# Kernel optimization log

Measured on AMD Instinct MI355X. Metric: run time of the kernel, lower is better.

## Reference

```python
import jax, jax.numpy as jnp
from jax import lax
import numpy as np

H, W, C = 128, 128, 1024          # backbone feature map (stride-16, ResNet C4)
STRIDE = 16
NUM_ANCHORS = 9                   # 3 scales x 3 ratios
IOU_THRESHOLD = 0.7
SCORE_THRESHOLD = 0.5


def _make_anchors():
    scales = np.array([128.0, 256.0, 512.0], np.float32)
    ratios = np.array([0.5, 1.0, 2.0], np.float32)
    hs = (scales[:, None] * np.sqrt(ratios)[None, :]).reshape(-1)   # [9]
    ws = (scales[:, None] / np.sqrt(ratios)[None, :]).reshape(-1)   # [9]
    cy = (np.arange(H, dtype=np.float32) + 0.5) * STRIDE
    cx = (np.arange(W, dtype=np.float32) + 0.5) * STRIDE
    anc = np.zeros((H, W, NUM_ANCHORS, 4), np.float32)
    anc[..., 0] = cy[:, None, None]
    anc[..., 1] = cx[None, :, None]
    anc[..., 2] = hs
    anc[..., 3] = ws
    return anc.reshape(-1, 4)      # [N,4] as (cy, cx, h, w)


def _conv(x, w, b):
    return lax.conv_general_dilated(
        x, w, (1, 1), 'SAME', dimension_numbers=('NHWC', 'HWIO', 'NHWC')) + b


def _rpn_head(features, w1, b1, w2, b2, w_score, b_score, w_box, b_box):
    x = jax.nn.relu(features)
    x = _conv(x, w1, b1)
    x = jax.nn.relu(x)
    x = _conv(x, w2, b2)
    scores = jax.nn.sigmoid(_conv(x, w_score, b_score))   # [1,H,W,9]
    shifts = _conv(x, w_box, b_box)                        # [1,H,W,36]
    return scores.reshape(-1, 1), shifts.reshape(-1, 4)


def _decode(shifts, anchors):
    acy, acx, ah, aw = anchors[:, 0], anchors[:, 1], anchors[:, 2], anchors[:, 3]
    dy, dx, dh, dw = shifts[:, 0], shifts[:, 1], shifts[:, 2], shifts[:, 3]
    cy = acy + dy * ah
    cx = acx + dx * aw
    h = ah * jnp.exp(dh)
    w = aw * jnp.exp(dw)
    y1 = jnp.clip(cy - 0.5 * h, 0.0, H * STRIDE)
    x1 = jnp.clip(cx - 0.5 * w, 0.0, W * STRIDE)
    y2 = jnp.clip(cy + 0.5 * h, 0.0, H * STRIDE)
    x2 = jnp.clip(cx + 0.5 * w, 0.0, W * STRIDE)
    return jnp.stack([y1, x1, y2, x2], axis=-1)            # [N,4]


def _nms(boxes, scores, max_out):
    """Greedy NMS like tf.image.non_max_suppression, fixed-size padded output."""
    n = boxes.shape[0]
    areas = (boxes[:, 2] - boxes[:, 0]) * (boxes[:, 3] - boxes[:, 1])

    def body(state):
        suppressed, sel, count = state
        masked = jnp.where(suppressed, -jnp.inf, scores)
        i = jnp.argmax(masked)
        valid = masked[i] >= SCORE_THRESHOLD
        sel = sel.at[count].set(jnp.where(valid, i.astype(jnp.int32), -1))
        count = count + valid.astype(jnp.int32)
        b = boxes[i]
        iy = jnp.maximum(0.0, jnp.minimum(b[2], boxes[:, 2]) - jnp.maximum(b[0], boxes[:, 0]))
        ix = jnp.maximum(0.0, jnp.minimum(b[3], boxes[:, 3]) - jnp.maximum(b[1], boxes[:, 1]))
        inter = iy * ix
        iou = inter / (areas[i] + areas - inter + 1e-9)
        new_sup = (suppressed | (iou > IOU_THRESHOLD)).at[i].set(True)
        suppressed = jnp.where(valid, new_sup, jnp.ones_like(suppressed))
        return suppressed, sel, count

    def cond(state):
        suppressed, sel, count = state
        return (count < max_out) & (~jnp.all(suppressed))

    sel0 = jnp.full((max_out,), -1, jnp.int32)
    sup0 = jnp.zeros((n,), bool)
    _, sel, _ = lax.while_loop(cond, body, (sup0, sel0, jnp.int32(0)))
    valid = sel >= 0
    idx = jnp.where(valid, sel, 0)
    return boxes[idx] * valid[:, None], scores[idx] * valid, valid


def setup_inputs() -> dict:
    key = jax.random.key(0)
    ks = jax.random.split(key, 5)
    def init_w(k, shape, fan_in, scale=1.0):
        return jax.random.normal(k, shape, jnp.float32) * (scale / np.sqrt(fan_in))
    features = jax.random.normal(ks[0], (1, H, W, C), jnp.float32)
    w1 = init_w(ks[1], (3, 3, C, 512), 9 * C)
    b1 = jnp.zeros((512,), jnp.float32)
    w2 = init_w(ks[2], (3, 3, 512, 512), 9 * 512)
    b2 = jnp.zeros((512,), jnp.float32)
    w_score = init_w(ks[3], (1, 1, 512, NUM_ANCHORS), 512)
    b_score = jnp.zeros((NUM_ANCHORS,), jnp.float32)
    w_box = init_w(ks[4], (1, 1, 512, 4 * NUM_ANCHORS), 512, scale=0.1)
    b_box = jnp.zeros((4 * NUM_ANCHORS,), jnp.float32)
    return {"features": features, "w1": w1, "b1": b1, "w2": w2, "b2": b2,
            "w_score": w_score, "b_score": b_score,
            "w_box": w_box, "b_box": b_box, "region_limit": 300}


def reference(features, w1, b1, w2, b2, w_score, b_score, w_box, b_box, region_limit):
    pred_scores, pred_shifts = _rpn_head(features, w1, b1, w2, b2,
                                         w_score, b_score, w_box, b_box)
    anchors = jnp.asarray(_make_anchors())
    boxes = _decode(pred_shifts, anchors)
    return _nms(boxes, pred_scores[:, 0], int(region_limit))
```

## Files before the change

kernel.cpp:

```cpp
#include <hip/hip_runtime.h>

#define HW 128
#define COUTC 512
#define NB 4097
#define NSEL 300
#define T_TOP 4096
#define TW 64

typedef _Float16 half8 __attribute__((ext_vector_type(8)));
typedef _Float16 half4v __attribute__((ext_vector_type(4)));
typedef float floatx4 __attribute__((ext_vector_type(4)));

#define NWS_A1H   ((size_t)0)
#define NWS_A1L   ((size_t)34611200)
#define NWS_W1H   ((size_t)69222400)
#define NWS_W1L   ((size_t)78659584)
#define NWS_A2H   ((size_t)88096768)
#define NWS_A2L   ((size_t)105402368)
#define NWS_W2H   ((size_t)122707968)
#define NWS_W2L   ((size_t)127426560)
#define NWS_X2    ((size_t)132145152)
#define NWS_BOXES ((size_t)165699584)
#define NWS_KEYS  ((size_t)168058880)
#define NWS_SKEYS ((size_t)169238528)
#define NWS_HIST  ((size_t)170418176)
#define NWS_CUR   ((size_t)170434816)
#define NWS_CNT   ((size_t)170451456)
#define NWS_BASE  ((size_t)170451712)
#define NWS_TOTAL ((size_t)170468352)

#define WS_X1     ((size_t)0)
#define WS_X2     ((size_t)33554432)
#define WS_BOXES  ((size_t)67108864)
#define WS_KEYS   ((size_t)69468160)
#define WS_SKEYS  ((size_t)70647808)
#define WS_HIST   ((size_t)71827456)
#define WS_CUR    ((size_t)71844096)
#define WS_CNT    ((size_t)71860736)
#define WS_BASE   ((size_t)71860992)

__device__ __forceinline__ void glds16(const void* g, void* l) {
    __builtin_amdgcn_global_load_lds(
        (const __attribute__((address_space(1))) void*)g,
        (__attribute__((address_space(3))) void*)l, 16, 0, 0);
}


__global__ __launch_bounds__(256) void convert_feat_kernel(
    const float* __restrict__ feat, _Float16* __restrict__ ah, _Float16* __restrict__ al)
{
    int p  = blockIdx.x;
    int pr = p / 130, pc = p % 130;
    int c  = threadIdx.x * 4;
    half4v vh = (half4v)(_Float16)0.f, vl = (half4v)(_Float16)0.f;
    if (pr != 0 && pr != 129 && pc != 0 && pc != 129) {
        float4 v = *(const float4*)&feat[(size_t)(((pr - 1) * HW) + (pc - 1)) * 1024 + c];
        float f[4] = {v.x, v.y, v.z, v.w};
        #pragma unroll
        for (int i = 0; i < 4; ++i) {
            float x = fmaxf(f[i], 0.f);
            _Float16 hi = (_Float16)x;
            vh[i] = hi;
            vl[i] = (_Float16)(x - (float)hi);
        }
    }
    size_t o = (size_t)pr * 133120 + (size_t)(c >> 5) * 4160
             + (size_t)((c >> 3) & 3) * 1040 + (size_t)pc * 8 + (c & 7);
    *(half4v*)&ah[o] = vh;
    *(half4v*)&al[o] = vl;
}

template<int CIN>
__device__ __forceinline__ void convert_w_body(
    int b, const float* __restrict__ w, _Float16* __restrict__ wh, _Float16* __restrict__ wl)
{
    constexpr int NU = CIN / 8;
    int gid = b * 256 + threadIdx.x;
    int oc = gid & 511;
    int rest = gid >> 9;
    int u = rest & (NU - 1);
    int tap = rest / NU;
    if (tap >= 9) return;
    int k0 = u * 8;
    half8 vh, vl;
    #pragma unroll
    for (int j = 0; j < 8; ++j) {
        float v = w[((size_t)tap * CIN + k0 + j) * 512 + oc] * 64.f;
        _Float16 hi = (_Float16)v;
        vh[j] = hi;
        vl[j] = (_Float16)(v - (float)hi);
    }
    size_t o = (size_t)tap * CIN * 512 + (size_t)(k0 >> 5) * 16384
             + (size_t)((k0 >> 3) & 3) * 4096 + (size_t)oc * 8;
    *(half8*)(wh + o) = vh;
    *(half8*)(wl + o) = vl;
}

__global__ __launch_bounds__(256) void prep_kernel(
    const float* __restrict__ w1, _Float16* __restrict__ w1h, _Float16* __restrict__ w1l,
    const float* __restrict__ w2, _Float16* __restrict__ w2h, _Float16* __restrict__ w2l,
    const float* __restrict__ w_s, const float* __restrict__ w_b,
    _Float16* __restrict__ wbh, _Float16* __restrict__ wbl,
    _Float16* __restrict__ a2h, _Float16* __restrict__ a2l)
{
    int b = blockIdx.x;
    if (b < 2304) { convert_w_body<1024>(b, w1, w1h, w1l); return; }
    if (b < 3456) { convert_w_body<512>(b - 2304, w2, w2h, w2l); return; }
    if (b < 3584) {
        int gid = (b - 3456) * 256 + threadIdx.x;
        int n = gid & 63;
        int k = gid >> 6;
        float v = 0.f;
        if (n < 9)       v = w_s[k * 9 + n] * 64.f;
        else if (n < 45) v = w_b[k * 36 + (n - 9)] * 64.f;
        _Float16 hi = (_Float16)v;
        size_t o = (size_t)(k >> 5) * 2048 + (size_t)((k >> 3) & 3) * 512 + (size_t)n * 8 + (k & 7);
        wbh[o] = hi;
        wbl[o] = (_Float16)(v - (float)hi);
        return;
    }
    {
        int i = b - 3584;
        int pr, pc;
        if (i < 130)      { pr = 0;        pc = i; }
        else if (i < 260) { pr = 129;      pc = i - 130; }
        else if (i < 388) { pr = i - 259;  pc = 0; }
        else              { pr = i - 387;  pc = 129; }
        int t = threadIdx.x;
        if (t >= 128) return;
        _Float16* dst = (t & 64) ? a2l : a2h;
        int u = t & 63;
        size_t o = (size_t)pr * 66560 + (size_t)(u >> 2) * 4160 + (size_t)(u & 3) * 1040 + (size_t)pc * 8;
        *(float4*)(dst + o) = make_float4(0.f, 0.f, 0.f, 0.f);
    }
}

template<int CIN, bool PAD>
__global__ __launch_bounds__(256) void conv_mfma_kernel(
    const _Float16* __restrict__ ah, const _Float16* __restrict__ al,
    const _Float16* __restrict__ wh, const _Float16* __restrict__ wl,
    const float* __restrict__ bias,
    _Float16* __restrict__ oh, _Float16* __restrict__ ol)
{
    constexpr int ROWSTR = CIN * 130;
    constexpr int TAPW   = CIN * 512;
    __shared__ __align__(16) _Float16 lds[32768];

    int bx = blockIdx.x;
    int h  = bx & 127;
    int n0 = (bx >> 7) << 7;

    int tid  = threadIdx.x;
    int wave = tid >> 6;
    int lane = tid & 63;
    int fr = lane & 15;
    int fq = lane >> 4;

    int aoff0 = fq * 1040 + (32 * wave + fr) * 8;
    int aoff1 = aoff0 + 128;
    int boff0 = fq * 4096 + (n0 + 32 * wave + fr) * 8;
    int boff1 = boff0 + 128;

    int wm = wave & 1, wn = wave >> 1;

    floatx4 acc[4][4];
    #pragma unroll
    for (int i = 0; i < 4; ++i)
        #pragma unroll
        for (int j = 0; j < 4; ++j)
            acc[i][j] = (floatx4){0.f, 0.f, 0.f, 0.f};

    #pragma unroll
    for (int tap = 0; tap < 9; ++tap) {
        int dy = tap / 3 - 1, dx = tap % 3 - 1;
        const _Float16* gAh = ah + (size_t)(h + dy + 1) * ROWSTR + (dx + 1) * 8;
        const _Float16* gAl = al + (size_t)(h + dy + 1) * ROWSTR + (dx + 1) * 8;
        const _Float16* gBh = wh + (size_t)tap * TAPW;
        const _Float16* gBl = wl + (size_t)tap * TAPW;

        for (int kc = 0; kc < CIN; kc += 64) {
            #pragma unroll
            for (int s = 0; s < 2; ++s) {
                int ab = ((kc >> 5) + s) * 4160;
                int bb = ((kc >> 5) + s) * 16384;
                _Float16* A0 = lds +          s * 4096 + 2 * wave * 512;
                _Float16* L0 = lds + 8192  +  s * 4096 + 2 * wave * 512;
                _Float16* B0 = lds + 16384 +  s * 4096 + 2 * wave * 512;
                _Float16* C0 = lds + 24576 +  s * 4096 + 2 * wave * 512;
                glds16(gAh + ab + aoff0, A0);
                glds16(gAh + ab + aoff1, A0 + 512);
                glds16(gAl + ab + aoff0, L0);
                glds16(gAl + ab + aoff1, L0 + 512);
                glds16(gBh + bb + boff0, B0);
                glds16(gBh + bb + boff1, B0 + 512);
                glds16(gBl + bb + boff0, C0);
                glds16(gBl + bb + boff1, C0 + 512);
            }
            __syncthreads();

            #pragma unroll
            for (int s = 0; s < 2; ++s) {
                const _Float16* rAh = lds +          s * 4096 + wm * 2048 + fq * 128 + fr * 8;
                const _Float16* rAl = rAh + 8192;
                const _Float16* rBh = lds + 16384 +  s * 4096 + wn * 2048 + fq * 128 + fr * 8;
                const _Float16* rBl = rBh + 8192;

                half8 fah[4], fal[4], fbh[4], fbl[4];
                #pragma unroll
                for (int i = 0; i < 4; ++i) {
                    fah[i] = *(const half8*)(rAh + i * 512);
                    fal[i] = *(const half8*)(rAl + i * 512);
                    fbh[i] = *(const half8*)(rBh + i * 512);
                    fbl[i] = *(const half8*)(rBl + i * 512);
                }
                #pragma unroll
                for (int i = 0; i < 4; ++i)
                    #pragma unroll
                    for (int j = 0; j < 4; ++j)
                        acc[i][j] = __builtin_amdgcn_mfma_f32_16x16x32_f16(fah[i], fbh[j], acc[i][j], 0, 0, 0);
                #pragma unroll
                for (int i = 0; i < 4; ++i)
                    #pragma unroll
                    for (int j = 0; j < 4; ++j)
                        acc[i][j] = __builtin_amdgcn_mfma_f32_16x16x32_f16(fah[i], fbl[j], acc[i][j], 0, 0, 0);
                #pragma unroll
                for (int i = 0; i < 4; ++i)
                    #pragma unroll
                    for (int j = 0; j < 4; ++j)
                        acc[i][j] = __builtin_amdgcn_mfma_f32_16x16x32_f16(fal[i], fbh[j], acc[i][j], 0, 0, 0);
            }
            __syncthreads();
        }
    }

    const float scale = 1.f / 64.f;
    int em = 64 * wm + fq * 4;
    int en = 64 * wn + fr;
    #pragma unroll
    for (int j = 0; j < 4; ++j) {
        int oc = n0 + en + 16 * j;
        float b = bias[oc];
        #pragma unroll
        for (int i = 0; i < 4; ++i) {
            #pragma unroll
            for (int r = 0; r < 4; ++r) {
                int w = em + 16 * i + r;
                float v = fmaf(acc[i][j][r], scale, b);
                if (PAD) {
                    v = fmaxf(v, 0.f);
                    _Float16 hi = (_Float16)v;
                    size_t o = (size_t)(h + 1) * 66560 + (size_t)(oc >> 5) * 4160
                             + (size_t)((oc >> 3) & 3) * 1040 + (size_t)(w + 1) * 8 + (oc & 7);
                    oh[o] = hi;
                    ol[o] = (_Float16)(v - (float)hi);
                } else {
                    _Float16 hi = (_Float16)v;
                    size_t o = (size_t)h * 65536 + (size_t)(oc >> 5) * 4096
                             + (size_t)((oc >> 3) & 3) * 1024 + (size_t)w * 8 + (oc & 7);
                    oh[o] = hi;
                    ol[o] = (_Float16)(v - (float)hi);
                }
            }
        }
    }
}

__device__ __forceinline__ void decode_emit(
    int gi, float z, float dyv, float dxv, float dhv, float dwv,
    float4* __restrict__ boxes, unsigned long long* __restrict__ keys,
    int* __restrict__ cnt, int* __restrict__ hist)
{
    int a = gi % 9;
    int pix = gi / 9;
    int h = pix >> 7, w = pix & 127;
    float sc  = (a < 3) ? 128.f : ((a < 6) ? 256.f : 512.f);
    int r = a - (a / 3) * 3;
    float ratio = (r == 0) ? 0.5f : ((r == 1) ? 1.f : 2.f);
    float sr = sqrtf(ratio);
    float ahh = sc * sr, aww = sc / sr;
    float acy = ((float)h + 0.5f) * 16.f;
    float acx = ((float)w + 0.5f) * 16.f;
    float cy = fmaf(dyv, ahh, acy);
    float cx = fmaf(dxv, aww, acx);
    float hh = ahh * expf(dhv);
    float ww = aww * expf(dwv);
    float y1 = fminf(fmaxf(cy - 0.5f * hh, 0.f), 2048.f);
    float x1 = fminf(fmaxf(cx - 0.5f * ww, 0.f), 2048.f);
    float y2 = fminf(fmaxf(cy + 0.5f * hh, 0.f), 2048.f);
    float x2 = fminf(fmaxf(cx + 0.5f * ww, 0.f), 2048.f);
    boxes[gi] = make_float4(y1, x1, y2, x2);
    float s = 1.f / (1.f + expf(-z));
    if (s >= 0.5f) {
        unsigned u = __float_as_uint(s);
        unsigned d = 0x3F800000u - u;
        unsigned long long key = ((unsigned long long)d << 18) | (unsigned)gi;
        int p = atomicAdd(cnt, 1);
        keys[p] = key;
        atomicAdd(&hist[d >> 11], 1);
    }
}

__global__ __launch_bounds__(256) void heads_mfma_kernel(
    const _Float16* __restrict__ xh, const _Float16* __restrict__ xl,
    const _Float16* __restrict__ wbh, const _Float16* __restrict__ wbl,
    const float* __restrict__ b_s, const float* __restrict__ b_b,
    float4* __restrict__ boxes, unsigned long long* __restrict__ keys,
    int* __restrict__ cnt, int* __restrict__ hist)
{
    __shared__ __align__(16) char smem[49152];
    _Float16* sAh = (_Float16*)smem;
    _Float16* sAl = (_Float16*)(smem + 16384);
    _Float16* sBh = (_Float16*)(smem + 32768);
    _Float16* sBl = (_Float16*)(smem + 40960);
    float* outs = (float*)smem;
    __shared__ float sb[48];

    int tid  = threadIdx.x;
    int wave = tid >> 6;
    int lane = tid & 63;
    int fr = lane & 15;
    int fq = lane >> 4;
    if (tid < 48) sb[tid] = (tid < 9) ? b_s[tid] : ((tid < 45) ? b_b[tid - 9] : 0.f);

    int h0 = blockIdx.x << 1;
    int rowsel = wave >> 1;
    int seg = (wave & 1) * 2048;

    floatx4 acc[4][3];
    #pragma unroll
    for (int i = 0; i < 4; ++i)
        #pragma unroll
        for (int j = 0; j < 3; ++j)
            acc[i][j] = (floatx4){0.f, 0.f, 0.f, 0.f};

    for (int kc = 0; kc < 16; ++kc) {
        const _Float16* gxh = xh + (size_t)(h0 + rowsel) * 65536 + kc * 4096 + seg;
        const _Float16* gxl = xl + (size_t)(h0 + rowsel) * 65536 + kc * 4096 + seg;
        _Float16* dAh = sAh + rowsel * 4096 + seg;
        _Float16* dAl = sAl + rowsel * 4096 + seg;
        #pragma unroll
        for (int q = 0; q < 4; ++q) {
            glds16(gxh + q * 512 + lane * 8, dAh + q * 512);
            glds16(gxl + q * 512 + lane * 8, dAl + q * 512);
        }
        glds16(wbh + kc * 2048 + wave * 512 + lane * 8, sBh + wave * 512);
        glds16(wbl + kc * 2048 + wave * 512 + lane * 8, sBl + wave * 512);
        __syncthreads();

        half8 fah[4], fal[4], fbh[3], fbl[3];
        #pragma unroll
        for (int i = 0; i < 4; ++i) {
            int pixLocal = wave * 64 + 16 * i + fr;
            int aaddr = (pixLocal >> 7) * 4096 + fq * 1024 + (pixLocal & 127) * 8;
            fah[i] = *(const half8*)(sAh + aaddr);
            fal[i] = *(const half8*)(sAl + aaddr);
        }
        #pragma unroll
        for (int j = 0; j < 3; ++j) {
            int baddr = fq * 512 + (16 * j + fr) * 8;
            fbh[j] = *(const half8*)(sBh + baddr);
            fbl[j] = *(const half8*)(sBl + baddr);
        }
        #pragma unroll
        for (int i = 0; i < 4; ++i)
            #pragma unroll
            for (int j = 0; j < 3; ++j) {
                acc[i][j] = __builtin_amdgcn_mfma_f32_16x16x32_f16(fah[i], fbh[j], acc[i][j], 0, 0, 0);
                acc[i][j] = __builtin_amdgcn_mfma_f32_16x16x32_f16(fah[i], fbl[j], acc[i][j], 0, 0, 0);
                acc[i][j] = __builtin_amdgcn_mfma_f32_16x16x32_f16(fal[i], fbh[j], acc[i][j], 0, 0, 0);
            }
        __syncthreads();
    }

    const float scale = 1.f / 64.f;
    #pragma unroll
    for (int i = 0; i < 4; ++i)
        #pragma unroll
        for (int j = 0; j < 3; ++j)
            #pragma unroll
            for (int r = 0; r < 4; ++r) {
                int pixLocal = wave * 64 + 16 * i + fq * 4 + r;
                int n = 16 * j + fr;
                if (n < 48)
                    outs[pixLocal * 48 + n] = fmaf(acc[i][j][r], scale, sb[n]);
            }
    __syncthreads();

    int p = tid;
    #pragma unroll
    for (int a = 0; a < 9; ++a) {
        float z   = outs[p * 48 + a];
        float dyv = outs[p * 48 + 9 + 4 * a + 0];
        float dxv = outs[p * 48 + 9 + 4 * a + 1];
        float dhv = outs[p * 48 + 9 + 4 * a + 2];
        float dwv = outs[p * 48 + 9 + 4 * a + 3];
        int gi = (h0 * 128 + p) * 9 + a;
        decode_emit(gi, z, dyv, dxv, dhv, dwv, boxes, keys, cnt, hist);
    }
}

template<int CIN, bool RELU_IN, bool RELU_OUT>
__global__ __launch_bounds__(256) void conv3x3_kernel(
    const float* __restrict__ in, const float* __restrict__ wgt,
    const float* __restrict__ bias, float* __restrict__ out)
{
    __shared__ float As[32][68];
    __shared__ float Bs[32][64];
    int bx = blockIdx.x;
    int mtile = bx & 255, ntile = bx >> 8;
    int h = mtile >> 1, w0 = (mtile & 1) << 6, n0 = ntile << 6;
    int tid = threadIdx.x, ty = tid >> 4, tx = tid & 15;
    float acc[4][4] = {{0.f}};
    const int KTOT = 9 * CIN;
    for (int k0 = 0; k0 < KTOT; k0 += 32) {
        int tap = k0 / CIN, icb = k0 % CIN;
        int dy = tap / 3 - 1, dx = tap % 3 - 1;
        int row = h + dy;
        bool rowok = ((unsigned)row < HW);
        {
            int pix = tid >> 3, cs = (tid & 7) << 2;
            #pragma unroll
            for (int p = 0; p < 2; ++p) {
                int px = pix + p * 32;
                int wcol = w0 + px + dx;
                float4 v = make_float4(0.f, 0.f, 0.f, 0.f);
                if (rowok && (unsigned)wcol < HW) {
                    v = *(const float4*)&in[((size_t)row * HW + wcol) * CIN + icb + cs];
                    if (RELU_IN) {
                        v.x = fmaxf(v.x, 0.f); v.y = fmaxf(v.y, 0.f);
                        v.z = fmaxf(v.z, 0.f); v.w = fmaxf(v.w, 0.f);
                    }
                }
                As[cs + 0][px] = v.x; As[cs + 1][px] = v.y;
                As[cs + 2][px] = v.z; As[cs + 3][px] = v.w;
            }
        }
        {
            int kr = tid >> 4, nc = (tid & 15) << 2;
            #pragma unroll
            for (int p = 0; p < 2; ++p) {
                int k = kr + p * 16;
                *(float4*)&Bs[k][nc] = *(const float4*)&wgt[(size_t)(k0 + k) * COUTC + n0 + nc];
            }
        }
        __syncthreads();
        #pragma unroll
        for (int kk = 0; kk < 32; ++kk) {
            float4 a = *(const float4*)&As[kk][ty << 2];
            float4 b = *(const float4*)&Bs[kk][tx << 2];
            float av[4] = {a.x, a.y, a.z, a.w};
            float bv[4] = {b.x, b.y, b.z, b.w};
            #pragma unroll
            for (int i = 0; i < 4; ++i)
                #pragma unroll
                for (int j = 0; j < 4; ++j)
                    acc[i][j] = fmaf(av[i], bv[j], acc[i][j]);
        }
        __syncthreads();
    }
    float4 bi = *(const float4*)&bias[n0 + (tx << 2)];
    float bv2[4] = {bi.x, bi.y, bi.z, bi.w};
    #pragma unroll
    for (int i = 0; i < 4; ++i) {
        float4 o;
        o.x = acc[i][0] + bv2[0]; o.y = acc[i][1] + bv2[1];
        o.z = acc[i][2] + bv2[2]; o.w = acc[i][3] + bv2[3];
        if (RELU_OUT) {
            o.x = fmaxf(o.x, 0.f); o.y = fmaxf(o.y, 0.f);
            o.z = fmaxf(o.z, 0.f); o.w = fmaxf(o.w, 0.f);
        }
        *(float4*)&out[((size_t)(h * HW) + w0 + (ty << 2) + i) * COUTC + n0 + (tx << 2)] = o;
    }
}

__global__ __launch_bounds__(256) void heads_decode_kernel(
    const float* __restrict__ x, const float* __restrict__ w_s, const float* __restrict__ b_s,
    const float* __restrict__ w_b, const float* __restrict__ b_b,
    float4* __restrict__ boxes, unsigned long long* __restrict__ keys,
    int* __restrict__ cnt, int* __restrict__ hist)
{
    __shared__ float xs[4][512];
    __shared__ float outs[4][45];
    int wave = threadIdx.x >> 6;
    int lane = threadIdx.x & 63;
    int pix  = blockIdx.x * 4 + wave;

    const float4* xp = (const float4*)&x[(size_t)pix * COUTC];
    *(float4*)&xs[wave][lane * 4]       = xp[lane];
    *(float4*)&xs[wave][256 + lane * 4] = xp[64 + lane];
    __syncthreads();

    if (lane < 45) {
        const float* wp; int stride; float acc;
        if (lane < 9) { wp = w_s + lane;       stride = 9;  acc = b_s[lane]; }
        else          { wp = w_b + (lane - 9); stride = 36; acc = b_b[lane - 9]; }
        const float* xrow = xs[wave];
        for (int k = 0; k < 512; k += 4) {
            acc = fmaf(xrow[k + 0], wp[(k + 0) * stride], acc);
            acc = fmaf(xrow[k + 1], wp[(k + 1) * stride], acc);
            acc = fmaf(xrow[k + 2], wp[(k + 2) * stride], acc);
            acc = fmaf(xrow[k + 3], wp[(k + 3) * stride], acc);
        }
        outs[wave][lane] = acc;
    }
    __syncthreads();

    if (lane < 9) {
        int a = lane;
        decode_emit(pix * 9 + a, outs[wave][a],
                    outs[wave][9 + 4 * a + 0], outs[wave][9 + 4 * a + 1],
                    outs[wave][9 + 4 * a + 2], outs[wave][9 + 4 * a + 3],
                    boxes, keys, cnt, hist);
    }
}

__global__ __launch_bounds__(256) void scan_kernel(
    const int* __restrict__ hist, int* __restrict__ base)
{
    __shared__ int buf[256];
    __shared__ int carry;
    int tid = threadIdx.x;
    if (tid == 0) carry = 0;
    __syncthreads();
    for (int c = 0; c < NB; c += 256) {
        int idx = c + tid;
        int v = (idx < NB) ? hist[idx] : 0;
        buf[tid] = v;
        __syncthreads();
        for (int s = 1; s < 256; s <<= 1) {
            int t = (tid >= s) ? buf[tid - s] : 0;
            __syncthreads();
            buf[tid] += t;
            __syncthreads();
        }
        if (idx < NB) base[idx] = carry + buf[tid] - v;
        __syncthreads();
        if (tid == 0) carry += buf[255];
        __syncthreads();
    }
    if (tid == 0) base[NB] = carry;
}

__global__ __launch_bounds__(256) void scatter_kernel(
    const unsigned long long* __restrict__ keys, const int* __restrict__ cnt,
    const int* __restrict__ base, int* __restrict__ cur,
    unsigned long long* __restrict__ skeys)
{
    int i = blockIdx.x * 256 + threadIdx.x;
    if (i < *cnt) {
        unsigned long long k = keys[i];
        int b = (int)(k >> 29);
        int p = base[b] + atomicAdd(&cur[b], 1);
        skeys[p] = k;
    }
}

__global__ __launch_bounds__(256) void sortb_kernel(
    const unsigned long long* __restrict__ skeys, const int* __restrict__ base,
    const float4* __restrict__ boxes,
    unsigned long long* __restrict__ sk2,
    float4* __restrict__ cboxes, float* __restrict__ careas)
{
    __shared__ unsigned long long sk[2048];
    int b = blockIdx.x;
    int s0 = base[b];
    int n = base[b + 1] - s0;
    if (n <= 0) return;
    int t = threadIdx.x;
    if (n <= 2048) {
        for (int i = t; i < n; i += 256) sk[i] = skeys[s0 + i];
        __syncthreads();
        for (int i = t; i < n; i += 256) {
            unsigned long long k = sk[i];
            int r = 0;
            for (int j = 0; j < n; ++j) r += (sk[j] < k) ? 1 : 0;
            int pos = s0 + r;
            sk2[pos] = k;
            if (pos < T_TOP) {
                float4 bb = boxes[k & 0x3FFFFull];
                cboxes[pos] = bb;
                careas[pos] = (bb.z - bb.x) * (bb.w - bb.y);
            }
        }
    } else {
        const unsigned long long* src = skeys + s0;
        for (int i = t; i < n; i += 256) {
            unsigned long long k = src[i];
            int r = 0;
            for (int j = 0; j < n; ++j) r += (src[j] < k) ? 1 : 0;
            int pos = s0 + r;
            sk2[pos] = k;
            if (pos < T_TOP) {
                float4 bb = boxes[k & 0x3FFFFull];
                cboxes[pos] = bb;
                careas[pos] = (bb.z - bb.x) * (bb.w - bb.y);
            }
        }
    }
}

__global__ __launch_bounds__(256) void mask_kernel(
    const float4* __restrict__ cboxes, const float* __restrict__ careas,
    unsigned long long* __restrict__ msk)
{
    int bi = blockIdx.y, bj = blockIdx.x;
    if (bj < bi) return;
    __shared__ float4 jb[256];
    __shared__ float  ja[256];
    int t = threadIdx.x;
    int j0 = bj << 8;
    jb[t] = cboxes[j0 + t];
    ja[t] = careas[j0 + t];
    __syncthreads();
    int i = (bi << 8) + t;
    float4 ci = cboxes[i];
    float ca = careas[i];
    unsigned long long word = 0;
    for (int jj = 0; jj < 256; ++jj) {
        int j = j0 + jj;
        float4 b = jb[jj];
        float iy = fmaxf(0.f, fminf(ci.z, b.z) - fmaxf(ci.x, b.x));
        float ix = fmaxf(0.f, fminf(ci.w, b.w) - fmaxf(ci.y, b.y));
        float inter = iy * ix;
        float iou = inter / (ca + ja[jj] - inter + 1e-9f);
        bool bit = (j == i) || (j > i && iou > 0.7f);
        if (bit) word |= 1ull << (jj & 63);
        if ((jj & 63) == 63) {
            msk[(size_t)i * TW + (bj << 2) + (jj >> 6)] = word;
            word = 0;
        }
    }
}

__global__ __launch_bounds__(64) void walk_kernel(
    const unsigned long long* __restrict__ sk2, const int* __restrict__ cnt,
    const float4* __restrict__ cboxes, const float* __restrict__ careas,
    const unsigned long long* __restrict__ msk, const float4* __restrict__ boxes,
    float* __restrict__ out)
{
    __shared__ unsigned long long sup[TW];
    __shared__ float4 sbox[NSEL];
    __shared__ float  sarea[NSEL];
    int lane = threadIdx.x;
    for (int i = lane; i < 1800; i += 64) out[i] = 0.f;
    sup[lane] = 0ull;
    __syncthreads();

    int total = *cnt;
    int Tc = min(total, T_TOP);
    int sel = 0;

    auto scanFrom = [&](int p) -> int {
        if (p < 0 || p >= Tc) return -1;
        int w = p >> 6;
        unsigned long long f = (~sup[w]) & (~0ull << (p & 63));
        while (f == 0ull) {
            ++w;
            if (w >= TW) return -1;
            f = ~sup[w];
        }
        int c = (w << 6) + __builtin_ctzll(f);
        return (c < Tc) ? c : -1;
    };

    unsigned long long r0, r1, r2n;
    int idx = scanFrom(0);
    if (idx >= 0) r0 = msk[(size_t)idx * TW + lane];
    int idx2 = (idx >= 0) ? scanFrom(idx + 1) : -1;
    if (idx2 >= 0) r1 = msk[(size_t)idx2 * TW + lane];

    while (idx >= 0 && sel < NSEL) {
        float4 cb = cboxes[idx];
        float ca = careas[idx];
        if (lane == 0) {
            unsigned long long key = sk2[idx];
            out[sel * 4 + 0] = cb.x; out[sel * 4 + 1] = cb.y;
            out[sel * 4 + 2] = cb.z; out[sel * 4 + 3] = cb.w;
            out[1200 + sel] = __uint_as_float(0x3F800000u - (unsigned)(key >> 18));
            out[1500 + sel] = 1.f;
            sbox[sel] = cb;
            sarea[sel] = ca;
        }
        sel++;
        if (sel >= NSEL) break;

        int idx3 = (idx2 >= 0) ? scanFrom(idx2 + 1) : -1;
        if (idx3 >= 0) r2n = msk[(size_t)idx3 * TW + lane];

        sup[lane] |= r0;
        __syncthreads();

        if (idx2 >= 0) {
            unsigned long long w = sup[idx2 >> 6];
            if ((w >> (idx2 & 63)) & 1ull) {
                idx2 = scanFrom(idx2);
                if (idx2 >= 0) r1 = msk[(size_t)idx2 * TW + lane];
                idx3 = (idx2 >= 0) ? scanFrom(idx2 + 1) : -1;
                if (idx3 >= 0) r2n = msk[(size_t)idx3 * TW + lane];
            }
        }
        idx = idx2; r0 = r1;
        idx2 = idx3; r1 = r2n;
    }

    if (sel < NSEL && total > T_TOP) {
        for (int i = T_TOP; i < total && sel < NSEL; ++i) {
            unsigned long long key = sk2[i];
            float4 cb = boxes[key & 0x3FFFFull];
            float ca = (cb.z - cb.x) * (cb.w - cb.y);
            int supp = 0;
            for (int t = lane; t < sel; t += 64) {
                float4 s4 = sbox[t];
                float iy = fmaxf(0.f, fminf(s4.z, cb.z) - fmaxf(s4.x, cb.x));
                float ix = fmaxf(0.f, fminf(s4.w, cb.w) - fmaxf(s4.y, cb.y));
                float inter = iy * ix;
                float iou = inter / (sarea[t] + ca - inter + 1e-9f);
                if (iou > 0.7f) supp = 1;
            }
            if (__ballot(supp) == 0ull) {
                if (lane == 0) {
                    out[sel * 4 + 0] = cb.x; out[sel * 4 + 1] = cb.y;
                    out[sel * 4 + 2] = cb.z; out[sel * 4 + 3] = cb.w;
                    out[1200 + sel] = __uint_as_float(0x3F800000u - (unsigned)(key >> 18));
                    out[1500 + sel] = 1.f;
                    sbox[sel] = cb;
                    sarea[sel] = ca;
                }
                sel++;
            }
        }
    }
}

extern "C" void kernel_launch(void* const* d_in, const int* in_sizes, int n_in,
                              void* d_out, int out_size, void* d_ws, size_t ws_size,
                              hipStream_t stream) {
    const float* feat = (const float*)d_in[0];
    const float* w1   = (const float*)d_in[1];
    const float* b1   = (const float*)d_in[2];
    const float* w2   = (const float*)d_in[3];
    const float* b2   = (const float*)d_in[4];
    const float* w_s  = (const float*)d_in[5];
    const float* b_s  = (const float*)d_in[6];
    const float* w_b  = (const float*)d_in[7];
    const float* b_b  = (const float*)d_in[8];
    float* out = (float*)d_out;
    char* ws = (char*)d_ws;

    if (ws_size >= NWS_TOTAL) {
        _Float16* a1h = (_Float16*)(ws + NWS_A1H);
        _Float16* a1l = (_Float16*)(ws + NWS_A1L);
        _Float16* w1h = (_Float16*)(ws + NWS_W1H);
        _Float16* w1l = (_Float16*)(ws + NWS_W1L);
        _Float16* a2h = (_Float16*)(ws + NWS_A2H);
        _Float16* a2l = (_Float16*)(ws + NWS_A2L);
        _Float16* w2h = (_Float16*)(ws + NWS_W2H);
        _Float16* w2l = (_Float16*)(ws + NWS_W2L);
        _Float16* xh  = (_Float16*)(ws + NWS_X2);
        _Float16* xl  = (_Float16*)(ws + NWS_X2 + 16777216);
        float4* boxes = (float4*)(ws + NWS_BOXES);
        unsigned long long* keys  = (unsigned long long*)(ws + NWS_KEYS);
        unsigned long long* skeys = (unsigned long long*)(ws + NWS_SKEYS);
        int* hist = (int*)(ws + NWS_HIST);
        int* cur  = (int*)(ws + NWS_CUR);
        int* cnt  = (int*)(ws + NWS_CNT);
        int* base = (int*)(ws + NWS_BASE);
        _Float16* wbh = (_Float16*)(ws + NWS_SKEYS);
        _Float16* wbl = (_Float16*)(ws + NWS_SKEYS + 65536);
        unsigned long long* msk = (unsigned long long*)(ws + NWS_A1H);
        float4* cbox  = (float4*)(ws + NWS_A1L);
        float*  carea = (float*)(ws + NWS_A1L + 262144);
        unsigned long long* sk2 = keys;

        hipMemsetAsync(ws + NWS_HIST, 0, (NWS_CNT - NWS_HIST) + 256, stream);
        convert_feat_kernel<<<16900, 256, 0, stream>>>(feat, a1h, a1l);
        prep_kernel<<<4100, 256, 0, stream>>>(w1, w1h, w1l, w2, w2h, w2l,
                                              w_s, w_b, wbh, wbl, a2h, a2l);
        conv_mfma_kernel<1024, true ><<<512, 256, 0, stream>>>(a1h, a1l, w1h, w1l, b1, a2h, a2l);
        conv_mfma_kernel< 512, false><<<512, 256, 0, stream>>>(a2h, a2l, w2h, w2l, b2, xh, xl);
        heads_mfma_kernel<<<64, 256, 0, stream>>>(xh, xl, wbh, wbl, b_s, b_b, boxes, keys, cnt, hist);
        scan_kernel<<<1, 256, 0, stream>>>(hist, base);
        scatter_kernel<<<576, 256, 0, stream>>>(keys, cnt, base, cur, skeys);
        sortb_kernel<<<NB, 256, 0, stream>>>(skeys, base, boxes, sk2, cbox, carea);
        mask_kernel<<<dim3(16, 16), 256, 0, stream>>>(cbox, carea, msk);
        walk_kernel<<<1, 64, 0, stream>>>(sk2, cnt, cbox, carea, msk, boxes, out);
    } else {
        float* x1 = (float*)(ws + WS_X1);
        float* x2 = (float*)(ws + WS_X2);
        float4* boxes = (float4*)(ws + WS_BOXES);
        unsigned long long* keys  = (unsigned long long*)(ws + WS_KEYS);
        unsigned long long* skeys = (unsigned long long*)(ws + WS_SKEYS);
        int* hist = (int*)(ws + WS_HIST);
        int* cur  = (int*)(ws + WS_CUR);
        int* cnt  = (int*)(ws + WS_CNT);
        int* base = (int*)(ws + WS_BASE);
        unsigned long long* msk = (unsigned long long*)(ws + WS_X1);
        float4* cbox  = (float4*)(ws + WS_X2);
        float*  carea = (float*)(ws + WS_X2 + 262144);
        unsigned long long* sk2 = keys;

        hipMemsetAsync(ws + WS_HIST, 0, (WS_CNT - WS_HIST) + 256, stream);
        conv3x3_kernel<1024, true,  true ><<<2048, 256, 0, stream>>>(feat, w1, b1, x1);
        conv3x3_kernel< 512, false, false><<<2048, 256, 0, stream>>>(x1,   w2, b2, x2);
        heads_decode_kernel<<<4096, 256, 0, stream>>>(x2, w_s, b_s, w_b, b_b, boxes, keys, cnt, hist);
        scan_kernel<<<1, 256, 0, stream>>>(hist, base);
        scatter_kernel<<<576, 256, 0, stream>>>(keys, cnt, base, cur, skeys);
        sortb_kernel<<<NB, 256, 0, stream>>>(skeys, base, boxes, sk2, cbox, carea);
        mask_kernel<<<dim3(16, 16), 256, 0, stream>>>(cbox, carea, msk);
        walk_kernel<<<1, 64, 0, stream>>>(sk2, cnt, cbox, carea, msk, boxes, out);
    }
}
```

Measured before the change: 1.015 ms.

## Rework feature conversion, heads tiling, scan, and NMS walk with LDS mask

Feature conversion now stages each row and channel chunk in shared memory so that global reads are coalesced per channel and writes go out as vectors. The heads kernel processes one row per block with a 2x2 wave split, doubling the block count and halving LDS per block. The scan becomes a single-pass per-thread chunk scan. The NMS walk preloads the first 1024 mask rows into LDS, finds candidates with a ballot-based search, and falls back to the old pipelined walk for the remainder. Together these aim to cut serial latency in the walk and improve occupancy in the small kernels, at the cost of a large 128KB LDS footprint in the single walk block.

```diff
diff --git a/kernel.cpp b/kernel.cpp
--- a/kernel.cpp
+++ b/kernel.cpp
@@ -6,6 +6,7 @@
 #define NSEL 300
 #define T_TOP 4096
 #define TW 64
+#define FAST_N 1024
 
 typedef _Float16 half8 __attribute__((ext_vector_type(8)));
 typedef _Float16 half4v __attribute__((ext_vector_type(4)));
@@ -49,25 +50,40 @@
 __global__ __launch_bounds__(256) void convert_feat_kernel(
     const float* __restrict__ feat, _Float16* __restrict__ ah, _Float16* __restrict__ al)
 {
-    int p  = blockIdx.x;
-    int pr = p / 130, pc = p % 130;
-    int c  = threadIdx.x * 4;
-    half4v vh = (half4v)(_Float16)0.f, vl = (half4v)(_Float16)0.f;
-    if (pr != 0 && pr != 129 && pc != 0 && pc != 129) {
-        float4 v = *(const float4*)&feat[(size_t)(((pr - 1) * HW) + (pc - 1)) * 1024 + c];
-        float f[4] = {v.x, v.y, v.z, v.w};
-        #pragma unroll
-        for (int i = 0; i < 4; ++i) {
-            float x = fmaxf(f[i], 0.f);
+    __shared__ __align__(16) _Float16 lh[130 * 32];
+    __shared__ __align__(16) _Float16 ll[130 * 32];
+    int pr = blockIdx.x;
+    int chunk = blockIdx.y;
+    int t = threadIdx.x;
+    int c  = t & 31;
+    int pg = t >> 5;
+    bool interior = (pr >= 1 && pr <= 128);
+    if (interior) {
+        for (int px = pg; px < 128; px += 8) {
+            float x = feat[((size_t)(pr - 1) * 128 + px) * 1024 + chunk * 32 + c];
+            x = fmaxf(x, 0.f);
             _Float16 hi = (_Float16)x;
-            vh[i] = hi;
-            vl[i] = (_Float16)(x - (float)hi);
-        }
-    }
-    size_t o = (size_t)pr * 133120 + (size_t)(c >> 5) * 4160
-             + (size_t)((c >> 3) & 3) * 1040 + (size_t)pc * 8 + (c & 7);
-    *(half4v*)&ah[o] = vh;
-    *(half4v*)&al[o] = vl;
+            lh[(px + 1) * 32 + c] = hi;
+            ll[(px + 1) * 32 + c] = (_Float16)(x - (float)hi);
+        }
+    } else {
+        for (int px = pg; px < 128; px += 8) {
+            lh[(px + 1) * 32 + c] = (_Float16)0.f;
+            ll[(px + 1) * 32 + c] = (_Float16)0.f;
+        }
+    }
+    if (t < 32) {
+        lh[t] = (_Float16)0.f;          ll[t] = (_Float16)0.f;
+        lh[129 * 32 + t] = (_Float16)0.f; ll[129 * 32 + t] = (_Float16)0.f;
+    }
+    __syncthreads();
+    size_t base = (size_t)pr * 133120 + (size_t)chunk * 4160;
+    for (int i = t; i < 520; i += 256) {
+        int sub = i / 130;
+        int pc  = i - sub * 130;
+        *(float4*)&ah[base + sub * 1040 + pc * 8] = *(const float4*)&lh[pc * 32 + sub * 8];
+        *(float4*)&al[base + sub * 1040 + pc * 8] = *(const float4*)&ll[pc * 32 + sub * 8];
+    }
 }
 
 template<int CIN>
@@ -307,11 +323,11 @@
     float4* __restrict__ boxes, unsigned long long* __restrict__ keys,
     int* __restrict__ cnt, int* __restrict__ hist)
 {
-    __shared__ __align__(16) char smem[49152];
+    __shared__ __align__(16) char smem[24576];
     _Float16* sAh = (_Float16*)smem;
-    _Float16* sAl = (_Float16*)(smem + 16384);
-    _Float16* sBh = (_Float16*)(smem + 32768);
-    _Float16* sBl = (_Float16*)(smem + 40960);
+    _Float16* sAl = (_Float16*)(smem + 8192);
+    _Float16* sBh = (_Float16*)(smem + 16384);
+    _Float16* sBl = (_Float16*)(smem + 20480);
     float* outs = (float*)smem;
     __shared__ float sb[48];
 
@@ -322,49 +338,46 @@
     int fq = lane >> 4;
     if (tid < 48) sb[tid] = (tid < 9) ? b_s[tid] : ((tid < 45) ? b_b[tid - 9] : 0.f);
 
-    int h0 = blockIdx.x << 1;
-    int rowsel = wave >> 1;
-    int seg = (wave & 1) * 2048;
-
-    floatx4 acc[4][3];
+    int h = blockIdx.x;
+    int wm = wave & 1, wn = wave >> 1;
+
+    floatx4 acc[4][2];
     #pragma unroll
     for (int i = 0; i < 4; ++i)
         #pragma unroll
-        for (int j = 0; j < 3; ++j)
+        for (int j = 0; j < 2; ++j)
             acc[i][j] = (floatx4){0.f, 0.f, 0.f, 0.f};
 
     for (int kc = 0; kc < 16; ++kc) {
-        const _Float16* gxh = xh + (size_t)(h0 + rowsel) * 65536 + kc * 4096 + seg;
-        const _Float16* gxl = xl + (size_t)(h0 + rowsel) * 65536 + kc * 4096 + seg;
-        _Float16* dAh = sAh + rowsel * 4096 + seg;
-        _Float16* dAl = sAl + rowsel * 4096 + seg;
-        #pragma unroll
-        for (int q = 0; q < 4; ++q) {
-            glds16(gxh + q * 512 + lane * 8, dAh + q * 512);
-            glds16(gxl + q * 512 + lane * 8, dAl + q * 512);
-        }
-        glds16(wbh + kc * 2048 + wave * 512 + lane * 8, sBh + wave * 512);
-        glds16(wbl + kc * 2048 + wave * 512 + lane * 8, sBl + wave * 512);
+        const _Float16* gxh = xh + (size_t)h * 65536 + kc * 4096;
+        const _Float16* gxl = xl + (size_t)h * 65536 + kc * 4096;
+        glds16(gxh + tid * 8,        sAh + tid * 8);
+        glds16(gxh + 2048 + tid * 8, sAh + 2048 + tid * 8);
+        glds16(gxl + tid * 8,        sAl + tid * 8);
+        glds16(gxl + 2048 + tid * 8, sAl + 2048 + tid * 8);
+        glds16(wbh + kc * 2048 + tid * 8, sBh + tid * 8);
+        glds16(wbl + kc * 2048 + tid * 8, sBl + tid * 8);
         __syncthreads();
 
-        half8 fah[4], fal[4], fbh[3], fbl[3];
+        half8 fah[4], fal[4], fbh[2], fbl[2];
         #pragma unroll
         for (int i = 0; i < 4; ++i) {
-            int pixLocal = wave * 64 + 16 * i + fr;
-            int aaddr = (pixLocal >> 7) * 4096 + fq * 1024 + (pixLocal & 127) * 8;
+            int px = wm * 64 + 16 * i + fr;
+            int aaddr = fq * 1024 + px * 8;
             fah[i] = *(const half8*)(sAh + aaddr);
             fal[i] = *(const half8*)(sAl + aaddr);
         }
         #pragma unroll
-        for (int j = 0; j < 3; ++j) {
-            int baddr = fq * 512 + (16 * j + fr) * 8;
+        for (int j = 0; j < 2; ++j) {
+            int n = wn * 32 + 16 * j + fr;
+            int baddr = fq * 512 + n * 8;
             fbh[j] = *(const half8*)(sBh + baddr);
             fbl[j] = *(const half8*)(sBl + baddr);
         }
         #pragma unroll
         for (int i = 0; i < 4; ++i)
             #pragma unroll
-            for (int j = 0; j < 3; ++j) {
+            for (int j = 0; j < 2; ++j) {
                 acc[i][j] = __builtin_amdgcn_mfma_f32_16x16x32_f16(fah[i], fbh[j], acc[i][j], 0, 0, 0);
                 acc[i][j] = __builtin_amdgcn_mfma_f32_16x16x32_f16(fah[i], fbl[j], acc[i][j], 0, 0, 0);
                 acc[i][j] = __builtin_amdgcn_mfma_f32_16x16x32_f16(fal[i], fbh[j], acc[i][j], 0, 0, 0);
@@ -376,26 +389,28 @@
     #pragma unroll
     for (int i = 0; i < 4; ++i)
         #pragma unroll
-        for (int j = 0; j < 3; ++j)
+        for (int j = 0; j < 2; ++j)
             #pragma unroll
             for (int r = 0; r < 4; ++r) {
-                int pixLocal = wave * 64 + 16 * i + fq * 4 + r;
-                int n = 16 * j + fr;
+                int px = wm * 64 + 16 * i + fq * 4 + r;
+                int n = wn * 32 + 16 * j + fr;
                 if (n < 48)
-                    outs[pixLocal * 48 + n] = fmaf(acc[i][j][r], scale, sb[n]);
+                    outs[px * 48 + n] = fmaf(acc[i][j][r], scale, sb[n]);
             }
     __syncthreads();
 
-    int p = tid;
-    #pragma unroll
-    for (int a = 0; a < 9; ++a) {
-        float z   = outs[p * 48 + a];
-        float dyv = outs[p * 48 + 9 + 4 * a + 0];
-        float dxv = outs[p * 48 + 9 + 4 * a + 1];
-        float dhv = outs[p * 48 + 9 + 4 * a + 2];
-        float dwv = outs[p * 48 + 9 + 4 * a + 3];
-        int gi = (h0 * 128 + p) * 9 + a;
-        decode_emit(gi, z, dyv, dxv, dhv, dwv, boxes, keys, cnt, hist);
+    if (tid < 128) {
+        int p = tid;
+        #pragma unroll
+        for (int a = 0; a < 9; ++a) {
+            float z   = outs[p * 48 + a];
+            float dyv = outs[p * 48 + 9 + 4 * a + 0];
+            float dxv = outs[p * 48 + 9 + 4 * a + 1];
+            float dhv = outs[p * 48 + 9 + 4 * a + 2];
+            float dwv = outs[p * 48 + 9 + 4 * a + 3];
+            int gi = (h * 128 + p) * 9 + a;
+            decode_emit(gi, z, dyv, dxv, dhv, dwv, boxes, keys, cnt, hist);
+        }
     }
 }
 
@@ -517,28 +532,24 @@
 __global__ __launch_bounds__(256) void scan_kernel(
     const int* __restrict__ hist, int* __restrict__ base)
 {
-    __shared__ int buf[256];
-    __shared__ int carry;
-    int tid = threadIdx.x;
-    if (tid == 0) carry = 0;
+    __shared__ int tot[256];
+    int t = threadIdx.x;
+    int v[16];
+    int s = 0;
+    #pragma unroll
+    for (int i = 0; i < 16; ++i) { v[i] = hist[t * 16 + i]; s += v[i]; }
+    tot[t] = s;
     __syncthreads();
-    for (int c = 0; c < NB; c += 256) {
-        int idx = c + tid;
-        int v = (idx < NB) ? hist[idx] : 0;
-        buf[tid] = v;
+    for (int d = 1; d < 256; d <<= 1) {
+        int x = (t >= d) ? tot[t - d] : 0;
         __syncthreads();
-        for (int s = 1; s < 256; s <<= 1) {
-            int t = (tid >= s) ? buf[tid - s] : 0;
-            __syncthreads();
-            buf[tid] += t;
-            __syncthreads();
-        }
-        if (idx < NB) base[idx] = carry + buf[tid] - v;
+        tot[t] += x;
         __syncthreads();
-        if (tid == 0) carry += buf[255];
-        __syncthreads();
-    }
-    if (tid == 0) base[NB] = carry;
+    }
+    int excl = (t == 0) ? 0 : tot[t - 1];
+    #pragma unroll
+    for (int i = 0; i < 16; ++i) { base[t * 16 + i] = excl; excl += v[i]; }
+    if (t == 255) { base[4096] = excl; base[4097] = excl + hist[4096]; }
 }
 
 __global__ __launch_bounds__(256) void scatter_kernel(
@@ -632,75 +643,123 @@
     }
 }
 
-__global__ __launch_bounds__(64) void walk_kernel(
+__global__ __launch_bounds__(256) void walk_kernel(
     const unsigned long long* __restrict__ sk2, const int* __restrict__ cnt,
     const float4* __restrict__ cboxes, const float* __restrict__ careas,
     const unsigned long long* __restrict__ msk, const float4* __restrict__ boxes,
     float* __restrict__ out)
 {
+    __shared__ unsigned long long mlds[FAST_N * 16];
     __shared__ unsigned long long sup[TW];
     __shared__ float4 sbox[NSEL];
     __shared__ float  sarea[NSEL];
-    int lane = threadIdx.x;
-    for (int i = lane; i < 1800; i += 64) out[i] = 0.f;
-    sup[lane] = 0ull;
-    __syncthreads();
-
+    __shared__ unsigned short sellist[NSEL];
+    int tid = threadIdx.x;
+    for (int i = tid; i < 1800; i += 256) out[i] = 0.f;
     int total = *cnt;
     int Tc = min(total, T_TOP);
+    int FN = min(Tc, FAST_N);
+    for (int i = tid; i < FN * 16; i += 256) {
+        mlds[i] = msk[(size_t)(i >> 4) * TW + (i & 15)];
+    }
+    if (tid < TW) sup[tid] = 0ull;
+    __syncthreads();
+    if (tid >= 64) return;
+    int lane = tid;
     int sel = 0;
 
-    auto scanFrom = [&](int p) -> int {
-        if (p < 0 || p >= Tc) return -1;
-        int w = p >> 6;
-        unsigned long long f = (~sup[w]) & (~0ull << (p & 63));
-        while (f == 0ull) {
-            ++w;
-            if (w >= TW) return -1;
-            f = ~sup[w];
-        }
-        int c = (w << 6) + __builtin_ctzll(f);
-        return (c < Tc) ? c : -1;
-    };
-
-    unsigned long long r0, r1, r2n;
-    int idx = scanFrom(0);
-    if (idx >= 0) r0 = msk[(size_t)idx * TW + lane];
-    int idx2 = (idx >= 0) ? scanFrom(idx + 1) : -1;
-    if (idx2 >= 0) r1 = msk[(size_t)idx2 * TW + lane];
-
-    while (idx >= 0 && sel < NSEL) {
-        float4 cb = cboxes[idx];
-        float ca = careas[idx];
-        if (lane == 0) {
-            unsigned long long key = sk2[idx];
-            out[sel * 4 + 0] = cb.x; out[sel * 4 + 1] = cb.y;
-            out[sel * 4 + 2] = cb.z; out[sel * 4 + 3] = cb.w;
-            out[1200 + sel] = __uint_as_float(0x3F800000u - (unsigned)(key >> 18));
-            out[1500 + sel] = 1.f;
-            sbox[sel] = cb;
-            sarea[sel] = ca;
-        }
-        sel++;
-        if (sel >= NSEL) break;
-
-        int idx3 = (idx2 >= 0) ? scanFrom(idx2 + 1) : -1;
-        if (idx3 >= 0) r2n = msk[(size_t)idx3 * TW + lane];
-
-        sup[lane] |= r0;
-        __syncthreads();
-
-        if (idx2 >= 0) {
-            unsigned long long w = sup[idx2 >> 6];
-            if ((w >> (idx2 & 63)) & 1ull) {
-                idx2 = scanFrom(idx2);
-                if (idx2 >= 0) r1 = msk[(size_t)idx2 * TW + lane];
-                idx3 = (idx2 >= 0) ? scanFrom(idx2 + 1) : -1;
-                if (idx3 >= 0) r2n = msk[(size_t)idx3 * TW + lane];
-            }
-        }
-        idx = idx2; r0 = r1;
-        idx2 = idx3; r1 = r2n;
+    {
+        int p = 0;
+        while (sel < NSEL) {
+            int w0 = p >> 6;
+            unsigned long long m = 0;
+            if (lane < 16 && lane >= w0) {
+                m = ~sup[lane];
+                if (lane == w0) m &= (~0ull << (p & 63));
+            }
+            unsigned long long bal = __ballot(m != 0ull);
+            if (bal == 0ull) break;
+            int w = __builtin_ctzll(bal);
+            int bit = __shfl(m ? __builtin_ctzll(m) : 0, w);
+            int c = (w << 6) + bit;
+            if (c >= FN) break;
+            float4 cb = cboxes[c];
+            float ca = careas[c];
+            if (lane == 0) {
+                unsigned long long key = sk2[c];
+                out[sel * 4 + 0] = cb.x; out[sel * 4 + 1] = cb.y;
+                out[sel * 4 + 2] = cb.z; out[sel * 4 + 3] = cb.w;
+                out[1200 + sel] = __uint_as_float(0x3F800000u - (unsigned)(key >> 18));
+                out[1500 + sel] = 1.f;
+                sbox[sel] = cb;
+                sarea[sel] = ca;
+                sellist[sel] = (unsigned short)c;
+            }
+            sel++;
+            if (lane < 16) sup[lane] |= mlds[c * 16 + lane];
+            p = c + 1;
+        }
+    }
+
+    if (sel < NSEL && Tc > FN) {
+        unsigned long long acc = 0ull;
+        if (lane >= 16) {
+            for (int s = 0; s < sel; ++s)
+                acc |= msk[(size_t)sellist[s] * TW + lane];
+            sup[lane] = acc;
+        }
+
+        auto scanFrom = [&](int p) -> int {
+            if (p < 0 || p >= Tc) return -1;
+            int w = p >> 6;
+            unsigned long long f = (~sup[w]) & (~0ull << (p & 63));
+            while (f == 0ull) {
+                ++w;
+                if (w >= TW) return -1;
+                f = ~sup[w];
+            }
+            int c = (w << 6) + __builtin_ctzll(f);
+            return (c < Tc) ? c : -1;
+        };
+
+        unsigned long long r0 = 0, r1 = 0, r2n = 0;
+        int idx = scanFrom(FN);
+        if (idx >= 0) r0 = msk[(size_t)idx * TW + lane];
+        int idx2 = (idx >= 0) ? scanFrom(idx + 1) : -1;
+        if (idx2 >= 0) r1 = msk[(size_t)idx2 * TW + lane];
+
+        while (idx >= 0 && sel < NSEL) {
+            float4 cb = cboxes[idx];
+            float ca = careas[idx];
+            if (lane == 0) {
+                unsigned long long key = sk2[idx];
+                out[sel * 4 + 0] = cb.x; out[sel * 4 + 1] = cb.y;
+                out[sel * 4 + 2] = cb.z; out[sel * 4 + 3] = cb.w;
+                out[1200 + sel] = __uint_as_float(0x3F800000u - (unsigned)(key >> 18));
+                out[1500 + sel] = 1.f;
+                sbox[sel] = cb;
+                sarea[sel] = ca;
+            }
+            sel++;
+            if (sel >= NSEL) break;
+
+            int idx3 = (idx2 >= 0) ? scanFrom(idx2 + 1) : -1;
+            if (idx3 >= 0) r2n = msk[(size_t)idx3 * TW + lane];
+
+            sup[lane] |= r0;
+
+            if (idx2 >= 0) {
+                unsigned long long w = sup[idx2 >> 6];
+                if ((w >> (idx2 & 63)) & 1ull) {
+                    idx2 = scanFrom(idx2);
+                    if (idx2 >= 0) r1 = msk[(size_t)idx2 * TW + lane];
+                    idx3 = (idx2 >= 0) ? scanFrom(idx2 + 1) : -1;
+                    if (idx3 >= 0) r2n = msk[(size_t)idx3 * TW + lane];
+                }
+            }
+            idx = idx2; r0 = r1;
+            idx2 = idx3; r1 = r2n;
+        }
     }
 
     if (sel < NSEL && total > T_TOP) {
@@ -773,17 +832,17 @@
         unsigned long long* sk2 = keys;
 
         hipMemsetAsync(ws + NWS_HIST, 0, (NWS_CNT - NWS_HIST) + 256, stream);
-        convert_feat_kernel<<<16900, 256, 0, stream>>>(feat, a1h, a1l);
+        convert_feat_kernel<<<dim3(130, 32), 256, 0, stream>>>(feat, a1h, a1l);
         prep_kernel<<<4100, 256, 0, stream>>>(w1, w1h, w1l, w2, w2h, w2l,
                                               w_s, w_b, wbh, wbl, a2h, a2l);
         conv_mfma_kernel<1024, true ><<<512, 256, 0, stream>>>(a1h, a1l, w1h, w1l, b1, a2h, a2l);
         conv_mfma_kernel< 512, false><<<512, 256, 0, stream>>>(a2h, a2l, w2h, w2l, b2, xh, xl);
-        heads_mfma_kernel<<<64, 256, 0, stream>>>(xh, xl, wbh, wbl, b_s, b_b, boxes, keys, cnt, hist);
+        heads_mfma_kernel<<<128, 256, 0, stream>>>(xh, xl, wbh, wbl, b_s, b_b, boxes, keys, cnt, hist);
         scan_kernel<<<1, 256, 0, stream>>>(hist, base);
         scatter_kernel<<<576, 256, 0, stream>>>(keys, cnt, base, cur, skeys);
         sortb_kernel<<<NB, 256, 0, stream>>>(skeys, base, boxes, sk2, cbox, carea);
         mask_kernel<<<dim3(16, 16), 256, 0, stream>>>(cbox, carea, msk);
-        walk_kernel<<<1, 64, 0, stream>>>(sk2, cnt, cbox, carea, msk, boxes, out);
+        walk_kernel<<<1, 256, 0, stream>>>(sk2, cnt, cbox, carea, msk, boxes, out);
     } else {
         float* x1 = (float*)(ws + WS_X1);
         float* x2 = (float*)(ws + WS_X2);
@@ -807,6 +866,6 @@
         scatter_kernel<<<576, 256, 0, stream>>>(keys, cnt, base, cur, skeys);
         sortb_kernel<<<NB, 256, 0, stream>>>(skeys, base, boxes, sk2, cbox, carea);
         mask_kernel<<<dim3(16, 16), 256, 0, stream>>>(cbox, carea, msk);
-        walk_kernel<<<1, 64, 0, stream>>>(sk2, cnt, cbox, carea, msk, boxes, out);
-    }
-}
+        walk_kernel<<<1, 256, 0, stream>>>(sk2, cnt, cbox, carea, msk, boxes, out);
+    }
+}
```

After: 871.3 us. 1.16x faster.
